# Performance work log

Measured on AMD Instinct MI355X. Metric: run time of the kernel, lower is better.

## Reference

```python
import jax, jax.numpy as jnp
import numpy as np

B, T, V, E, H, C = 64, 512, 32000, 256, 512, 4

def setup_inputs() -> dict:
    key = jax.random.key(0)
    ks = jax.random.split(key, 8)
    s = 1.0 / np.sqrt(H)  # torch LSTM default init scale
    return {
        "x": jax.random.randint(ks[0], (B, T), 0, V),
        "emb": jax.random.normal(ks[1], (V, E), jnp.float32) * 0.1,
        "W_ih": jax.random.uniform(ks[2], (4 * H, E), jnp.float32, -s, s),
        "W_hh": jax.random.uniform(ks[3], (4 * H, H), jnp.float32, -s, s),
        "b_ih": jax.random.uniform(ks[4], (4 * H,), jnp.float32, -s, s),
        "b_hh": jax.random.uniform(ks[5], (4 * H,), jnp.float32, -s, s),
        "W_fc": jax.random.uniform(ks[6], (C, H), jnp.float32, -s, s),
        "b_fc": jax.random.uniform(ks[7], (C,), jnp.float32, -s, s),
    }

def _lstm_last_hidden(e, W_ih, W_hh, b_ih, b_hh):
    # e: [B,T,E]. Precompute input-side gate preactivations for all steps.
    xg = jnp.einsum('bte,ge->tbg', e, W_ih) + (b_ih + b_hh)  # [T,B,4H]
    h0 = jnp.zeros((e.shape[0], H), e.dtype)
    c0 = jnp.zeros((e.shape[0], H), e.dtype)

    def step(carry, xt):
        h, c = carry
        g = xt + h @ W_hh.T                       # [B,4H]
        i, f, gg, o = jnp.split(g, 4, axis=-1)    # torch gate order: i,f,g,o
        i = jax.nn.sigmoid(i)
        f = jax.nn.sigmoid(f)
        gg = jnp.tanh(gg)
        o = jax.nn.sigmoid(o)
        c = f * c + i * gg
        h = o * jnp.tanh(c)
        return (h, c), None

    (hT, _), _ = jax.lax.scan(step, (h0, c0), xg)
    return hT  # last hidden == lstm_out[:, -1, :] for unidirectional LSTM

def reference(x, emb, W_ih, W_hh, b_ih, b_hh, W_fc, b_fc):
    e = emb[x]                                    # [B,T,E] embedding lookup
    hT = _lstm_last_hidden(e, W_ih, W_hh, b_ih, b_hh)
    return hT @ W_fc.T + b_fc                     # [B,C] logits
```

## Files before the change

### kernel.cpp

```cpp
#include <hip/hip_runtime.h>
#include <hip/hip_bf16.h>

#define B_  64
#define T_  512
#define E_  256
#define H_  512
#define G4_ 2048
#define C_  4

typedef __attribute__((ext_vector_type(4))) float  f32x4;
typedef __attribute__((ext_vector_type(8))) __bf16 bf16x8;
typedef __attribute__((ext_vector_type(8))) short  short8;
typedef __attribute__((ext_vector_type(4))) short  s16x4;

union V16 { f32x4 f; bf16x8 b; short8 s; };

__device__ __forceinline__ float sigmoid_(float x) { return 1.0f / (1.0f + __expf(-x)); }
__device__ __forceinline__ float tanh_(float x)    { return 1.0f - 2.0f / (__expf(2.0f * x) + 1.0f); }

__device__ __forceinline__ short f2bf(float f) {
  union { float f; unsigned u; } v; v.f = f;
  return (short)((v.u + 0x7FFFu + ((v.u >> 16) & 1u)) >> 16);
}

__device__ __forceinline__ void store_short_llc(void* p, unsigned v) {
  asm volatile("global_store_short %0, %1, off sc0 sc1" :: "v"(p), "v"(v) : "memory");
}
__device__ __forceinline__ void store_dword_llc(void* p, float v) {
  asm volatile("global_store_dword %0, %1, off sc0 sc1" :: "v"(p), "v"(v) : "memory");
}
__device__ __forceinline__ f32x4 ld_b128_llc(const void* p) {
  f32x4 v;
  asm volatile("global_load_dwordx4 %0, %1, off sc0 sc1\n\ts_waitcnt vmcnt(0)"
               : "=&v"(v) : "v"(p) : "memory");
  return v;
}

__global__ __launch_bounds__(256, 1) void wih_conv(const float* __restrict__ W,
                                                   short* __restrict__ out) {
  const int i = (blockIdx.x * 256 + threadIdx.x) * 4;
  f32x4 v = *(const f32x4*)(W + i);
  s16x4 s;
  s[0] = f2bf(v[0]); s[1] = f2bf(v[1]); s[2] = f2bf(v[2]); s[3] = f2bf(v[3]);
  *(s16x4*)(out + i) = s;
}

union XgSmem {
  struct { int idx[B_]; short e[B_][E_ + 8]; } g;
  short o[4][64][136];
};

template<bool WBF16>
__global__ __launch_bounds__(256, 2) void xg_kernel(
    const int* __restrict__ x, const float* __restrict__ emb,
    const void* __restrict__ Wv,
    __hip_bfloat16* __restrict__ xg)
{
  const int t   = blockIdx.x;
  const int tid = threadIdx.x;
  __shared__ XgSmem sm;

  if (tid < B_) sm.g.idx[tid] = x[tid * T_ + t];
  __syncthreads();
  {
    int b = tid >> 2, ch = tid & 3;
    const float* src = emb + (size_t)sm.g.idx[b] * E_ + ch * 64;
    short* dst = &sm.g.e[b][ch * 64];
#pragma unroll
    for (int i = 0; i < 16; i++) {
      f32x4 v = *(const f32x4*)(src + i * 4);
      s16x4 s;
      s[0] = f2bf(v[0]); s[1] = f2bf(v[1]); s[2] = f2bf(v[2]); s[3] = f2bf(v[3]);
      *(s16x4*)(dst + i * 4) = s;
    }
  }
  __syncthreads();

  const int wv   = tid >> 6;
  const int lane = tid & 63;
  const int ln15 = lane & 15, quad = lane >> 4;

  V16 breg[4][8];
#pragma unroll
  for (int nt = 0; nt < 4; nt++)
#pragma unroll
    for (int ks = 0; ks < 8; ks++)
      breg[nt][ks].f = *(const f32x4*)(&sm.g.e[nt * 16 + ln15][quad * 8 + ks * 32]);
  __syncthreads();

  const int gbase = wv * 512;
  const size_t base_t = (size_t)t * (G4_ * B_);

  for (int q = 0; q < 4; q++) {
#pragma unroll
    for (int m8 = 0; m8 < 8; m8++) {
      const int mt = q * 8 + m8;
      V16 areg[8];
      if constexpr (WBF16) {
        const short* arow = (const short*)Wv + (size_t)(gbase + mt * 16 + ln15) * E_ + quad * 8;
#pragma unroll
        for (int ks = 0; ks < 8; ks++)
          areg[ks].f = *(const f32x4*)(arow + ks * 32);
      } else {
        const float* arow = (const float*)Wv + (size_t)(gbase + mt * 16 + ln15) * E_ + quad * 8;
#pragma unroll
        for (int ks = 0; ks < 8; ks++) {
          f32x4 lo = *(const f32x4*)(arow + ks * 32);
          f32x4 hi = *(const f32x4*)(arow + ks * 32 + 4);
          short8 s;
          s[0] = f2bf(lo[0]); s[1] = f2bf(lo[1]); s[2] = f2bf(lo[2]); s[3] = f2bf(lo[3]);
          s[4] = f2bf(hi[0]); s[5] = f2bf(hi[1]); s[6] = f2bf(hi[2]); s[7] = f2bf(hi[3]);
          areg[ks].s = s;
        }
      }

      f32x4 acc[4];
#pragma unroll
      for (int nt = 0; nt < 4; nt++) acc[nt] = (f32x4){0.f, 0.f, 0.f, 0.f};
#pragma unroll
      for (int ks = 0; ks < 8; ks++)
#pragma unroll
        for (int nt = 0; nt < 4; nt++)
          acc[nt] = __builtin_amdgcn_mfma_f32_16x16x32_bf16(areg[ks].b, breg[nt][ks].b, acc[nt], 0, 0, 0);

      const int dl = m8 * 16 + quad * 4;
#pragma unroll
      for (int nt = 0; nt < 4; nt++) {
        const int batch = nt * 16 + ln15;
        s16x4 sv;
#pragma unroll
        for (int r = 0; r < 4; r++) sv[r] = f2bf(acc[nt][r]);
        *(s16x4*)&sm.o[wv][batch][dl] = sv;
      }
    }

    const size_t qbase = base_t + ((size_t)wv << 15) + q * 128;
    const int chunk = lane & 15;
#pragma unroll
    for (int i = 0; i < 16; i++) {
      const int row = (lane >> 4) + i * 4;
      f32x4 v = *(const f32x4*)&sm.o[wv][row][chunk * 8];
      *(f32x4*)((short*)xg + qbase + ((size_t)row << 9) + chunk * 8) = v;
    }
  }
}

__global__ __launch_bounds__(512, 2) void lstm_kernel(
    const float* __restrict__ W_hh,
    const float* __restrict__ b_ih, const float* __restrict__ b_hh,
    const float* __restrict__ W_fc, const float* __restrict__ b_fc,
    const __hip_bfloat16* __restrict__ xg,
    unsigned int* flags, __hip_bfloat16* hbuf , float* hT,
    float* out)
{
  const int tid  = threadIdx.x;
  const int blk  = blockIdx.x;
  const int g    = blk & 7;
  const int pd   = blk >> 3;
  const int d0   = pd * 64;
  const int wv   = tid >> 6;
  const int lane = tid & 63;
  const int ln15 = lane & 15, quad = lane >> 4;

  __shared__ __hip_bfloat16 s_h[16][520];
  __shared__ float s_pre[4][8][68];

  const int gate  = wv >> 1;
  const int dhalf = (wv & 1) * 32;
  V16 areg[2][16];
#pragma unroll
  for (int tau = 0; tau < 2; tau++) {
    const int grow = gate * 512 + d0 + dhalf + tau * 16 + ln15;
    const float* ap = W_hh + (size_t)grow * H_ + quad * 8;
#pragma unroll
    for (int ks = 0; ks < 16; ks++) {
      f32x4 lo = *(const f32x4*)(ap + ks * 32);
      f32x4 hi = *(const f32x4*)(ap + ks * 32 + 4);
      short8 s;
      s[0] = f2bf(lo[0]); s[1] = f2bf(lo[1]); s[2] = f2bf(lo[2]); s[3] = f2bf(lo[3]);
      s[4] = f2bf(hi[0]); s[5] = f2bf(hi[1]); s[6] = f2bf(hi[2]); s[7] = f2bf(hi[3]);
      areg[tau][ks].s = s;
    }
  }

  const int nb = tid >> 6;
  const int nd = tid & 63;
  const int gb = g * 8 + nb;
  const int dg = d0 + nd;
  const float bias_i = b_ih[dg]        + b_hh[dg];
  const float bias_f = b_ih[512 + dg]  + b_hh[512 + dg];
  const float bias_g = b_ih[1024 + dg] + b_hh[1024 + dg];
  const float bias_o = b_ih[1536 + dg] + b_hh[1536 + dg];
  float c = 0.0f;
  const int myflag = g * 16 + pd;

  *(f32x4*)&s_h[8 + (tid >> 6)][(tid & 63) * 8] = (f32x4){0.f, 0.f, 0.f, 0.f};

  for (int t = 0; t < T_; t++) {
    const int cur = t & 1, nxt = cur ^ 1;

    const size_t xoff = (size_t)t * (G4_ * B_) + ((size_t)gb << 9) + dg;
    const __hip_bfloat16 xgi = xg[xoff];
    const __hip_bfloat16 xgf = xg[xoff + (1u << 15)];
    const __hip_bfloat16 xgg = xg[xoff + (2u << 15)];
    const __hip_bfloat16 xgo = xg[xoff + (3u << 15)];

    if (tid < 8) {
      const unsigned* fp = flags + g * 16 + tid;
      while (__hip_atomic_load(fp, __ATOMIC_RELAXED, __HIP_MEMORY_SCOPE_AGENT) < (unsigned)t) {}
    }
    __syncthreads();

    {
      const short* hbase = (const short*)hbuf + (size_t)cur * (B_ * H_) + (size_t)(g * 8) * H_;
      f32x4 va = ld_b128_llc(hbase + tid * 8);
      *(f32x4*)&s_h[tid >> 6][(tid & 63) * 8] = va;
    }
    __syncthreads();

    f32x4 acc0 = (f32x4){0.f, 0.f, 0.f, 0.f};
    f32x4 acc1 = (f32x4){0.f, 0.f, 0.f, 0.f};
#pragma unroll
    for (int ks = 0; ks < 16; ks++) {
      V16 b0;
      b0.f = *(const f32x4*)&s_h[ln15][quad * 8 + ks * 32];
      acc0 = __builtin_amdgcn_mfma_f32_16x16x32_bf16(areg[0][ks].b, b0.b, acc0, 0, 0, 0);
      acc1 = __builtin_amdgcn_mfma_f32_16x16x32_bf16(areg[1][ks].b, b0.b, acc1, 0, 0, 0);
    }

    if (ln15 < 8) {
      *(f32x4*)&s_pre[gate][ln15][dhalf + quad * 4]      = acc0;
      *(f32x4*)&s_pre[gate][ln15][dhalf + 16 + quad * 4] = acc1;
    }
    __syncthreads();

    {
      const float pi = s_pre[0][nb][nd] + bias_i + __bfloat162float(xgi);
      const float pf = s_pre[1][nb][nd] + bias_f + __bfloat162float(xgf);
      const float pg = s_pre[2][nb][nd] + bias_g + __bfloat162float(xgg);
      const float po = s_pre[3][nb][nd] + bias_o + __bfloat162float(xgo);
      const float i_ = sigmoid_(pi), f_ = sigmoid_(pf);
      const float g_ = tanh_(pg),    o_ = sigmoid_(po);
      c = f_ * c + i_ * g_;
      const float h = o_ * tanh_(c);
      if (t < T_ - 1) {
        store_short_llc((short*)hbuf + (size_t)nxt * (B_ * H_) + (size_t)gb * H_ + dg,
                        (unsigned)(unsigned short)f2bf(h));
      } else {
        store_dword_llc(hT + gb * H_ + dg, h);
      }
    }
    __syncthreads();

    if (tid == 0)
      __hip_atomic_store(&flags[myflag], (unsigned)(t + 1),
                         __ATOMIC_RELAXED, __HIP_MEMORY_SCOPE_AGENT);
  }

  if (blk == 0) {
    if (tid < 64)
      while (__hip_atomic_load(flags + (tid >> 3) * 16 + (tid & 7),
                               __ATOMIC_RELAXED, __HIP_MEMORY_SCOPE_AGENT) < (unsigned)T_) {}
    __builtin_amdgcn_fence(__ATOMIC_ACQUIRE, "agent");
    __syncthreads();
    for (int o = tid; o < B_ * C_; o += 512) {
      const int b = o >> 2, cl = o & 3;
      const f32x4* hr = (const f32x4*)(hT + b * H_);
      const f32x4* wr = (const f32x4*)(W_fc + cl * H_);
      float s = 0.f;
      for (int d4 = 0; d4 < H_ / 4; d4++) {
        const f32x4 hv = hr[d4];
        const f32x4 wv4 = wr[d4];
        s += hv[0] * wv4[0] + hv[1] * wv4[1] + hv[2] * wv4[2] + hv[3] * wv4[3];
      }
      s += b_fc[cl];
      out[o] = s;
    }
  }
}

extern "C" void kernel_launch(void* const* d_in, const int* in_sizes, int n_in,
                              void* d_out, int out_size, void* d_ws, size_t ws_size,
                              hipStream_t stream) {
  const int*   x    = (const int*)d_in[0];
  const float* emb  = (const float*)d_in[1];
  const float* W_ih = (const float*)d_in[2];
  const float* W_hh = (const float*)d_in[3];
  const float* b_ih = (const float*)d_in[4];
  const float* b_hh = (const float*)d_in[5];
  const float* W_fc = (const float*)d_in[6];
  const float* b_fc = (const float*)d_in[7];
  float* out = (float*)d_out;

  char* ws = (char*)d_ws;
  const size_t XG_OFF  = 524288;
  const size_t XG_END  = XG_OFF + (size_t)T_ * G4_ * B_ * 2;
  const size_t NEEDED2 = XG_END + (size_t)G4_ * E_ * 2;
  if (ws_size < XG_END) return;

  unsigned int*   flags = (unsigned int*)ws;
  __hip_bfloat16* hbuf  = (__hip_bfloat16*)(ws + 4096);
  float*          hT    = (float*)(ws + 135168);
  __hip_bfloat16* xg    = (__hip_bfloat16*)(ws + XG_OFF);
  short*          wih16 = (short*)(ws + XG_END);

  (void)hipMemsetAsync(ws, 0, 135168, stream);

  if (ws_size >= NEEDED2) {
    wih_conv<<<512, 256, 0, stream>>>(W_ih, wih16);
    xg_kernel<true><<<T_, 256, 0, stream>>>(x, emb, wih16, xg);
  } else {
    xg_kernel<false><<<T_, 256, 0, stream>>>(x, emb, W_ih, xg);
  }
  lstm_kernel<<<64, 512, 0, stream>>>(W_hh, b_ih, b_hh, W_fc, b_fc, xg,
                                      flags, hbuf, hT, out);
}
```

Measured before the change: 1.263 ms.

## Process 16 batch rows per LSTM block, halving the persistent grid to 32 blocks

Each persistent LSTM block now handles 16 batch rows instead of 8, using all 16 columns of the MFMA B-operand that were previously zero-padded. The grid shrinks from 64 to 32 blocks, so each step needs fewer inter-block flag waits and fewer blocks participate in the cross-block synchronization. The trade-off is twice the gate elementwise work and xg loads per thread on each step, which lengthens the serial critical path per timestep.

```diff
diff --git a/kernel.cpp b/kernel.cpp
--- a/kernel.cpp
+++ b/kernel.cpp
@@ -29,11 +29,12 @@
 __device__ __forceinline__ void store_dword_llc(void* p, float v) {
   asm volatile("global_store_dword %0, %1, off sc0 sc1" :: "v"(p), "v"(v) : "memory");
 }
-__device__ __forceinline__ f32x4 ld_b128_llc(const void* p) {
-  f32x4 v;
-  asm volatile("global_load_dwordx4 %0, %1, off sc0 sc1\n\ts_waitcnt vmcnt(0)"
-               : "=&v"(v) : "v"(p) : "memory");
-  return v;
+__device__ __forceinline__ void ld2_b128_llc2(const void* p0, const void* p1,
+                                              f32x4& a, f32x4& b) {
+  asm volatile("global_load_dwordx4 %0, %2, off sc0 sc1\n\t"
+               "global_load_dwordx4 %1, %3, off sc0 sc1\n\t"
+               "s_waitcnt vmcnt(0)"
+               : "=&v"(a), "=&v"(b) : "v"(p0), "v"(p1) : "memory");
 }
 
 __global__ __launch_bounds__(256, 1) void wih_conv(const float* __restrict__ W,
@@ -155,15 +156,15 @@
 {
   const int tid  = threadIdx.x;
   const int blk  = blockIdx.x;
-  const int g    = blk & 7;
-  const int pd   = blk >> 3;
+  const int g    = blk & 3;
+  const int pd   = blk >> 2;
   const int d0   = pd * 64;
   const int wv   = tid >> 6;
   const int lane = tid & 63;
   const int ln15 = lane & 15, quad = lane >> 4;
 
   __shared__ __hip_bfloat16 s_h[16][520];
-  __shared__ float s_pre[4][8][68];
+  __shared__ float s_pre[4][16][68];
 
   const int gate  = wv >> 1;
   const int dhalf = (wv & 1) * 32;
@@ -185,25 +186,28 @@
 
   const int nb = tid >> 6;
   const int nd = tid & 63;
-  const int gb = g * 8 + nb;
+  const int gb = g * 16 + nb;
   const int dg = d0 + nd;
   const float bias_i = b_ih[dg]        + b_hh[dg];
   const float bias_f = b_ih[512 + dg]  + b_hh[512 + dg];
   const float bias_g = b_ih[1024 + dg] + b_hh[1024 + dg];
   const float bias_o = b_ih[1536 + dg] + b_hh[1536 + dg];
-  float c = 0.0f;
+  float c0 = 0.0f, c1 = 0.0f;
   const int myflag = g * 16 + pd;
-
-  *(f32x4*)&s_h[8 + (tid >> 6)][(tid & 63) * 8] = (f32x4){0.f, 0.f, 0.f, 0.f};
 
   for (int t = 0; t < T_; t++) {
     const int cur = t & 1, nxt = cur ^ 1;
 
-    const size_t xoff = (size_t)t * (G4_ * B_) + ((size_t)gb << 9) + dg;
-    const __hip_bfloat16 xgi = xg[xoff];
-    const __hip_bfloat16 xgf = xg[xoff + (1u << 15)];
-    const __hip_bfloat16 xgg = xg[xoff + (2u << 15)];
-    const __hip_bfloat16 xgo = xg[xoff + (3u << 15)];
+    const size_t xoff  = (size_t)t * (G4_ * B_) + ((size_t)gb << 9) + dg;
+    const size_t xoff2 = xoff + (8u << 9);
+    const __hip_bfloat16 xgi0 = xg[xoff];
+    const __hip_bfloat16 xgf0 = xg[xoff + (1u << 15)];
+    const __hip_bfloat16 xgg0 = xg[xoff + (2u << 15)];
+    const __hip_bfloat16 xgo0 = xg[xoff + (3u << 15)];
+    const __hip_bfloat16 xgi1 = xg[xoff2];
+    const __hip_bfloat16 xgf1 = xg[xoff2 + (1u << 15)];
+    const __hip_bfloat16 xgg1 = xg[xoff2 + (2u << 15)];
+    const __hip_bfloat16 xgo1 = xg[xoff2 + (3u << 15)];
 
     if (tid < 8) {
       const unsigned* fp = flags + g * 16 + tid;
@@ -212,9 +216,11 @@
     __syncthreads();
 
     {
-      const short* hbase = (const short*)hbuf + (size_t)cur * (B_ * H_) + (size_t)(g * 8) * H_;
-      f32x4 va = ld_b128_llc(hbase + tid * 8);
-      *(f32x4*)&s_h[tid >> 6][(tid & 63) * 8] = va;
+      const short* hbase = (const short*)hbuf + (size_t)cur * (B_ * H_) + (size_t)(g * 16) * H_;
+      f32x4 va, vb;
+      ld2_b128_llc2(hbase + tid * 8, hbase + 4096 + tid * 8, va, vb);
+      *(f32x4*)&s_h[tid >> 6][(tid & 63) * 8]       = va;
+      *(f32x4*)&s_h[8 + (tid >> 6)][(tid & 63) * 8] = vb;
     }
     __syncthreads();
 
@@ -228,26 +234,37 @@
       acc1 = __builtin_amdgcn_mfma_f32_16x16x32_bf16(areg[1][ks].b, b0.b, acc1, 0, 0, 0);
     }
 
-    if (ln15 < 8) {
-      *(f32x4*)&s_pre[gate][ln15][dhalf + quad * 4]      = acc0;
-      *(f32x4*)&s_pre[gate][ln15][dhalf + 16 + quad * 4] = acc1;
-    }
+    *(f32x4*)&s_pre[gate][ln15][dhalf + quad * 4]      = acc0;
+    *(f32x4*)&s_pre[gate][ln15][dhalf + 16 + quad * 4] = acc1;
     __syncthreads();
 
     {
-      const float pi = s_pre[0][nb][nd] + bias_i + __bfloat162float(xgi);
-      const float pf = s_pre[1][nb][nd] + bias_f + __bfloat162float(xgf);
-      const float pg = s_pre[2][nb][nd] + bias_g + __bfloat162float(xgg);
-      const float po = s_pre[3][nb][nd] + bias_o + __bfloat162float(xgo);
-      const float i_ = sigmoid_(pi), f_ = sigmoid_(pf);
-      const float g_ = tanh_(pg),    o_ = sigmoid_(po);
-      c = f_ * c + i_ * g_;
-      const float h = o_ * tanh_(c);
+      const float pi0 = s_pre[0][nb][nd] + bias_i + __bfloat162float(xgi0);
+      const float pf0 = s_pre[1][nb][nd] + bias_f + __bfloat162float(xgf0);
+      const float pg0 = s_pre[2][nb][nd] + bias_g + __bfloat162float(xgg0);
+      const float po0 = s_pre[3][nb][nd] + bias_o + __bfloat162float(xgo0);
+      const float i0 = sigmoid_(pi0), f0 = sigmoid_(pf0);
+      const float g0 = tanh_(pg0),    o0 = sigmoid_(po0);
+      c0 = f0 * c0 + i0 * g0;
+      const float h0 = o0 * tanh_(c0);
+      const float pi1 = s_pre[0][8 + nb][nd] + bias_i + __bfloat162float(xgi1);
+      const float pf1 = s_pre[1][8 + nb][nd] + bias_f + __bfloat162float(xgf1);
+      const float pg1 = s_pre[2][8 + nb][nd] + bias_g + __bfloat162float(xgg1);
+      const float po1 = s_pre[3][8 + nb][nd] + bias_o + __bfloat162float(xgo1);
+      const float i1 = sigmoid_(pi1), f1 = sigmoid_(pf1);
+      const float g1 = tanh_(pg1),    o1 = sigmoid_(po1);
+      c1 = f1 * c1 + i1 * g1;
+      const float h1 = o1 * tanh_(c1);
+
       if (t < T_ - 1) {
-        store_short_llc((short*)hbuf + (size_t)nxt * (B_ * H_) + (size_t)gb * H_ + dg,
-                        (unsigned)(unsigned short)f2bf(h));
+        short* sb = (short*)hbuf + (size_t)nxt * (B_ * H_);
+        store_short_llc(sb + (size_t)gb * H_ + dg,
+                        (unsigned)(unsigned short)f2bf(h0));
+        store_short_llc(sb + (size_t)(gb + 8) * H_ + dg,
+                        (unsigned)(unsigned short)f2bf(h1));
       } else {
-        store_dword_llc(hT + gb * H_ + dg, h);
+        store_dword_llc(hT + gb * H_ + dg, h0);
+        store_dword_llc(hT + (gb + 8) * H_ + dg, h1);
       }
     }
     __syncthreads();
@@ -258,7 +275,7 @@
   }
 
   if (blk == 0) {
-    if (tid < 64)
+    if (tid < 32)
       while (__hip_atomic_load(flags + (tid >> 3) * 16 + (tid & 7),
                                __ATOMIC_RELAXED, __HIP_MEMORY_SCOPE_AGENT) < (unsigned)T_) {}
     __builtin_amdgcn_fence(__ATOMIC_ACQUIRE, "agent");
@@ -312,6 +329,6 @@
   } else {
     xg_kernel<false><<<T_, 256, 0, stream>>>(x, emb, W_ih, xg);
   }
-  lstm_kernel<<<64, 512, 0, stream>>>(W_hh, b_ih, b_hh, W_fc, b_fc, xg,
+  lstm_kernel<<<32, 512, 0, stream>>>(W_hh, b_ih, b_hh, W_fc, b_fc, xg,
                                       flags, hbuf, hT, out);
 }
```

After: 1.498 ms. 18.6% more time.

## Fuse input projection and embedding gather into persistent LSTM kernel

Applied to the files above, without the earlier changes.

Removes the separate W_ih conversion and xg precompute kernels. Each LSTM block now holds its W_ih slice in registers as bf16 and computes the input-side gate preactivations per step with MFMA before waiting on the recurrence flags. The next step's embedding row is prefetched into a double-buffered shared tile. This avoids writing and reading the large xg buffer and two kernel launches, but adds MFMA work and register pressure (launch bounds drop to one block per CU) inside the serial loop.

```diff
diff --git a/kernel.cpp b/kernel.cpp
--- a/kernel.cpp
+++ b/kernel.cpp
@@ -36,120 +36,11 @@
   return v;
 }
 
-__global__ __launch_bounds__(256, 1) void wih_conv(const float* __restrict__ W,
-                                                   short* __restrict__ out) {
-  const int i = (blockIdx.x * 256 + threadIdx.x) * 4;
-  f32x4 v = *(const f32x4*)(W + i);
-  s16x4 s;
-  s[0] = f2bf(v[0]); s[1] = f2bf(v[1]); s[2] = f2bf(v[2]); s[3] = f2bf(v[3]);
-  *(s16x4*)(out + i) = s;
-}
-
-union XgSmem {
-  struct { int idx[B_]; short e[B_][E_ + 8]; } g;
-  short o[4][64][136];
-};
-
-template<bool WBF16>
-__global__ __launch_bounds__(256, 2) void xg_kernel(
+__global__ __launch_bounds__(512, 1) void lstm_kernel(
     const int* __restrict__ x, const float* __restrict__ emb,
-    const void* __restrict__ Wv,
-    __hip_bfloat16* __restrict__ xg)
-{
-  const int t   = blockIdx.x;
-  const int tid = threadIdx.x;
-  __shared__ XgSmem sm;
-
-  if (tid < B_) sm.g.idx[tid] = x[tid * T_ + t];
-  __syncthreads();
-  {
-    int b = tid >> 2, ch = tid & 3;
-    const float* src = emb + (size_t)sm.g.idx[b] * E_ + ch * 64;
-    short* dst = &sm.g.e[b][ch * 64];
-#pragma unroll
-    for (int i = 0; i < 16; i++) {
-      f32x4 v = *(const f32x4*)(src + i * 4);
-      s16x4 s;
-      s[0] = f2bf(v[0]); s[1] = f2bf(v[1]); s[2] = f2bf(v[2]); s[3] = f2bf(v[3]);
-      *(s16x4*)(dst + i * 4) = s;
-    }
-  }
-  __syncthreads();
-
-  const int wv   = tid >> 6;
-  const int lane = tid & 63;
-  const int ln15 = lane & 15, quad = lane >> 4;
-
-  V16 breg[4][8];
-#pragma unroll
-  for (int nt = 0; nt < 4; nt++)
-#pragma unroll
-    for (int ks = 0; ks < 8; ks++)
-      breg[nt][ks].f = *(const f32x4*)(&sm.g.e[nt * 16 + ln15][quad * 8 + ks * 32]);
-  __syncthreads();
-
-  const int gbase = wv * 512;
-  const size_t base_t = (size_t)t * (G4_ * B_);
-
-  for (int q = 0; q < 4; q++) {
-#pragma unroll
-    for (int m8 = 0; m8 < 8; m8++) {
-      const int mt = q * 8 + m8;
-      V16 areg[8];
-      if constexpr (WBF16) {
-        const short* arow = (const short*)Wv + (size_t)(gbase + mt * 16 + ln15) * E_ + quad * 8;
-#pragma unroll
-        for (int ks = 0; ks < 8; ks++)
-          areg[ks].f = *(const f32x4*)(arow + ks * 32);
-      } else {
-        const float* arow = (const float*)Wv + (size_t)(gbase + mt * 16 + ln15) * E_ + quad * 8;
-#pragma unroll
-        for (int ks = 0; ks < 8; ks++) {
-          f32x4 lo = *(const f32x4*)(arow + ks * 32);
-          f32x4 hi = *(const f32x4*)(arow + ks * 32 + 4);
-          short8 s;
-          s[0] = f2bf(lo[0]); s[1] = f2bf(lo[1]); s[2] = f2bf(lo[2]); s[3] = f2bf(lo[3]);
-          s[4] = f2bf(hi[0]); s[5] = f2bf(hi[1]); s[6] = f2bf(hi[2]); s[7] = f2bf(hi[3]);
-          areg[ks].s = s;
-        }
-      }
-
-      f32x4 acc[4];
-#pragma unroll
-      for (int nt = 0; nt < 4; nt++) acc[nt] = (f32x4){0.f, 0.f, 0.f, 0.f};
-#pragma unroll
-      for (int ks = 0; ks < 8; ks++)
-#pragma unroll
-        for (int nt = 0; nt < 4; nt++)
-          acc[nt] = __builtin_amdgcn_mfma_f32_16x16x32_bf16(areg[ks].b, breg[nt][ks].b, acc[nt], 0, 0, 0);
-
-      const int dl = m8 * 16 + quad * 4;
-#pragma unroll
-      for (int nt = 0; nt < 4; nt++) {
-        const int batch = nt * 16 + ln15;
-        s16x4 sv;
-#pragma unroll
-        for (int r = 0; r < 4; r++) sv[r] = f2bf(acc[nt][r]);
-        *(s16x4*)&sm.o[wv][batch][dl] = sv;
-      }
-    }
-
-    const size_t qbase = base_t + ((size_t)wv << 15) + q * 128;
-    const int chunk = lane & 15;
-#pragma unroll
-    for (int i = 0; i < 16; i++) {
-      const int row = (lane >> 4) + i * 4;
-      f32x4 v = *(const f32x4*)&sm.o[wv][row][chunk * 8];
-      *(f32x4*)((short*)xg + qbase + ((size_t)row << 9) + chunk * 8) = v;
-    }
-  }
-}
-
-__global__ __launch_bounds__(512, 2) void lstm_kernel(
-    const float* __restrict__ W_hh,
+    const float* __restrict__ W_ih, const float* __restrict__ W_hh,
     const float* __restrict__ b_ih, const float* __restrict__ b_hh,
     const float* __restrict__ W_fc, const float* __restrict__ b_fc,
-    const __hip_bfloat16* __restrict__ xg,
     unsigned int* flags, __hip_bfloat16* hbuf , float* hT,
     float* out)
 {
@@ -164,22 +55,40 @@
 
   __shared__ __hip_bfloat16 s_h[16][520];
   __shared__ float s_pre[4][8][68];
+  __shared__ __hip_bfloat16 s_e[2][16][264];
 
   const int gate  = wv >> 1;
   const int dhalf = (wv & 1) * 32;
-  V16 areg[2][16];
+  const int grow  = gate * 512 + d0 + dhalf;
+
+  V16 aregH[2][16];
+  V16 aregI[2][8];
 #pragma unroll
   for (int tau = 0; tau < 2; tau++) {
-    const int grow = gate * 512 + d0 + dhalf + tau * 16 + ln15;
-    const float* ap = W_hh + (size_t)grow * H_ + quad * 8;
-#pragma unroll
-    for (int ks = 0; ks < 16; ks++) {
-      f32x4 lo = *(const f32x4*)(ap + ks * 32);
-      f32x4 hi = *(const f32x4*)(ap + ks * 32 + 4);
-      short8 s;
-      s[0] = f2bf(lo[0]); s[1] = f2bf(lo[1]); s[2] = f2bf(lo[2]); s[3] = f2bf(lo[3]);
-      s[4] = f2bf(hi[0]); s[5] = f2bf(hi[1]); s[6] = f2bf(hi[2]); s[7] = f2bf(hi[3]);
-      areg[tau][ks].s = s;
+    const int r = grow + tau * 16 + ln15;
+    {
+      const float* ap = W_hh + (size_t)r * H_ + quad * 8;
+#pragma unroll
+      for (int ks = 0; ks < 16; ks++) {
+        f32x4 lo = *(const f32x4*)(ap + ks * 32);
+        f32x4 hi = *(const f32x4*)(ap + ks * 32 + 4);
+        short8 s;
+        s[0] = f2bf(lo[0]); s[1] = f2bf(lo[1]); s[2] = f2bf(lo[2]); s[3] = f2bf(lo[3]);
+        s[4] = f2bf(hi[0]); s[5] = f2bf(hi[1]); s[6] = f2bf(hi[2]); s[7] = f2bf(hi[3]);
+        aregH[tau][ks].s = s;
+      }
+    }
+    {
+      const float* ap = W_ih + (size_t)r * E_ + quad * 8;
+#pragma unroll
+      for (int ks = 0; ks < 8; ks++) {
+        f32x4 lo = *(const f32x4*)(ap + ks * 32);
+        f32x4 hi = *(const f32x4*)(ap + ks * 32 + 4);
+        short8 s;
+        s[0] = f2bf(lo[0]); s[1] = f2bf(lo[1]); s[2] = f2bf(lo[2]); s[3] = f2bf(lo[3]);
+        s[4] = f2bf(hi[0]); s[5] = f2bf(hi[1]); s[6] = f2bf(hi[2]); s[7] = f2bf(hi[3]);
+        aregI[tau][ks].s = s;
+      }
     }
   }
 
@@ -194,16 +103,39 @@
   float c = 0.0f;
   const int myflag = g * 16 + pd;
 
-  *(f32x4*)&s_h[8 + (tid >> 6)][(tid & 63) * 8] = (f32x4){0.f, 0.f, 0.f, 0.f};
+  *(f32x4*)&s_h[8 + wv][lane * 8] = (f32x4){0.f, 0.f, 0.f, 0.f};
+  {
+    const int buf = tid >> 8, row = 8 + ((tid >> 5) & 7), col = (tid & 31) * 8;
+    short8 z = (short8){0,0,0,0,0,0,0,0};
+    *(short8*)&s_e[buf][row][col] = z;
+  }
+  {
+    const int idx0 = x[gb * T_ + 0];
+    f32x4 v = *(const f32x4*)(emb + (size_t)idx0 * E_ + nd * 4);
+    s16x4 sv;
+    sv[0] = f2bf(v[0]); sv[1] = f2bf(v[1]); sv[2] = f2bf(v[2]); sv[3] = f2bf(v[3]);
+    *(s16x4*)&s_e[0][nb][nd * 4] = sv;
+  }
+  __syncthreads();
 
   for (int t = 0; t < T_; t++) {
     const int cur = t & 1, nxt = cur ^ 1;
 
-    const size_t xoff = (size_t)t * (G4_ * B_) + ((size_t)gb << 9) + dg;
-    const __hip_bfloat16 xgi = xg[xoff];
-    const __hip_bfloat16 xgf = xg[xoff + (1u << 15)];
-    const __hip_bfloat16 xgg = xg[xoff + (2u << 15)];
-    const __hip_bfloat16 xgo = xg[xoff + (3u << 15)];
+    f32x4 acc0 = (f32x4){0.f, 0.f, 0.f, 0.f};
+    f32x4 acc1 = (f32x4){0.f, 0.f, 0.f, 0.f};
+#pragma unroll
+    for (int ks = 0; ks < 8; ks++) {
+      V16 b0;
+      b0.f = *(const f32x4*)&s_e[cur][ln15][quad * 8 + ks * 32];
+      acc0 = __builtin_amdgcn_mfma_f32_16x16x32_bf16(aregI[0][ks].b, b0.b, acc0, 0, 0, 0);
+      acc1 = __builtin_amdgcn_mfma_f32_16x16x32_bf16(aregI[1][ks].b, b0.b, acc1, 0, 0, 0);
+    }
+
+    f32x4 ev;
+    if (t + 1 < T_) {
+      const int idx1 = x[gb * T_ + t + 1];
+      ev = *(const f32x4*)(emb + (size_t)idx1 * E_ + nd * 4);
+    }
 
     if (tid < 8) {
       const unsigned* fp = flags + g * 16 + tid;
@@ -218,14 +150,12 @@
     }
     __syncthreads();
 
-    f32x4 acc0 = (f32x4){0.f, 0.f, 0.f, 0.f};
-    f32x4 acc1 = (f32x4){0.f, 0.f, 0.f, 0.f};
 #pragma unroll
     for (int ks = 0; ks < 16; ks++) {
       V16 b0;
       b0.f = *(const f32x4*)&s_h[ln15][quad * 8 + ks * 32];
-      acc0 = __builtin_amdgcn_mfma_f32_16x16x32_bf16(areg[0][ks].b, b0.b, acc0, 0, 0, 0);
-      acc1 = __builtin_amdgcn_mfma_f32_16x16x32_bf16(areg[1][ks].b, b0.b, acc1, 0, 0, 0);
+      acc0 = __builtin_amdgcn_mfma_f32_16x16x32_bf16(aregH[0][ks].b, b0.b, acc0, 0, 0, 0);
+      acc1 = __builtin_amdgcn_mfma_f32_16x16x32_bf16(aregH[1][ks].b, b0.b, acc1, 0, 0, 0);
     }
 
     if (ln15 < 8) {
@@ -235,10 +165,10 @@
     __syncthreads();
 
     {
-      const float pi = s_pre[0][nb][nd] + bias_i + __bfloat162float(xgi);
-      const float pf = s_pre[1][nb][nd] + bias_f + __bfloat162float(xgf);
-      const float pg = s_pre[2][nb][nd] + bias_g + __bfloat162float(xgg);
-      const float po = s_pre[3][nb][nd] + bias_o + __bfloat162float(xgo);
+      const float pi = s_pre[0][nb][nd] + bias_i;
+      const float pf = s_pre[1][nb][nd] + bias_f;
+      const float pg = s_pre[2][nb][nd] + bias_g;
+      const float po = s_pre[3][nb][nd] + bias_o;
       const float i_ = sigmoid_(pi), f_ = sigmoid_(pf);
       const float g_ = tanh_(pg),    o_ = sigmoid_(po);
       c = f_ * c + i_ * g_;
@@ -249,6 +179,12 @@
       } else {
         store_dword_llc(hT + gb * H_ + dg, h);
       }
+    }
+
+    if (t + 1 < T_) {
+      s16x4 sv;
+      sv[0] = f2bf(ev[0]); sv[1] = f2bf(ev[1]); sv[2] = f2bf(ev[2]); sv[3] = f2bf(ev[3]);
+      *(s16x4*)&s_e[nxt][nb][nd * 4] = sv;
     }
     __syncthreads();
 
@@ -293,25 +229,14 @@
   float* out = (float*)d_out;
 
   char* ws = (char*)d_ws;
-  const size_t XG_OFF  = 524288;
-  const size_t XG_END  = XG_OFF + (size_t)T_ * G4_ * B_ * 2;
-  const size_t NEEDED2 = XG_END + (size_t)G4_ * E_ * 2;
-  if (ws_size < XG_END) return;
+  if (ws_size < 266240) return;
 
   unsigned int*   flags = (unsigned int*)ws;
   __hip_bfloat16* hbuf  = (__hip_bfloat16*)(ws + 4096);
   float*          hT    = (float*)(ws + 135168);
-  __hip_bfloat16* xg    = (__hip_bfloat16*)(ws + XG_OFF);
-  short*          wih16 = (short*)(ws + XG_END);
 
   (void)hipMemsetAsync(ws, 0, 135168, stream);
 
-  if (ws_size >= NEEDED2) {
-    wih_conv<<<512, 256, 0, stream>>>(W_ih, wih16);
-    xg_kernel<true><<<T_, 256, 0, stream>>>(x, emb, wih16, xg);
-  } else {
-    xg_kernel<false><<<T_, 256, 0, stream>>>(x, emb, W_ih, xg);
-  }
-  lstm_kernel<<<64, 512, 0, stream>>>(W_hh, b_ih, b_hh, W_fc, b_fc, xg,
-                                      flags, hbuf, hT, out);
-}
+  lstm_kernel<<<64, 512, 0, stream>>>(x, emb, W_ih, W_hh, b_ih, b_hh,
+                                      W_fc, b_fc, flags, hbuf, hT, out);
+}
```

Result: slower. 1.433 ms (+13.5%).
